# Kernel optimization log

Hardware: AMD Instinct MI355X
Metric: run time of the kernel (lower is better)

The kernel has to match this reference:

```python
import jax, jax.numpy as jnp
import numpy as np

# AAA hyperparameters (init_kwargs)
ALPHA = 1.0
TAU = 6.0
KAPPA = 100
T_TEMP = 1.0
BETA = 5.0
LR = 0.1
# torch.optim.AdamW defaults
B1, B2, EPS, WD = 0.9, 0.999, 1e-8, 0.01

B, D, C = 4096, 2048, 1000


def setup_inputs() -> dict:
    key = jax.random.key(0)
    kx, kw, kb = jax.random.split(key, 3)
    x = jax.random.normal(kx, (B, D), dtype=jnp.float32)
    W = jax.random.normal(kw, (D, C), dtype=jnp.float32) * 0.02  # linear classifier weight
    b = jax.random.normal(kb, (C,), dtype=jnp.float32) * 0.01
    return {"x": x, "W": W, "b": b}


def _ce(logits, y):
    # per-sample cross-entropy (nn.CrossEntropyLoss(reduce=False))
    return jax.nn.logsumexp(logits, axis=1) - jnp.take_along_axis(logits, y[:, None], axis=1)[:, 0]


def reference(x, W, b):
    # model inference under torch.no_grad(); z is detached in AAA
    z = jax.lax.stop_gradient(x @ W + b)  # [B, C]
    y = jnp.argmax(z, axis=1)             # pred_y, constant indices

    l_org = _ce(z, y)                                            # [B]
    l_atr = (jnp.floor(l_org / TAU) + 0.5) * TAU                 # [B]
    # AAA_type == 'sin'
    l_trg = l_org - ALPHA * TAU * jnp.sin(jnp.pi * (1.0 - 2.0 * (l_org - l_atr) / TAU))
    p_trg = jnp.max(jax.nn.softmax(z / T_TEMP, axis=1), axis=1)  # [B]

    def loss_fn(u):
        term1 = jnp.abs(_ce(u, y) - l_trg)                       # [B]
        # NOTE: torch.max(F.softmax(u, dim=1)) has NO dim arg -> GLOBAL max scalar,
        # broadcast against p_trg [B]. Faithful to the source.
        term2 = BETA * jnp.abs(jnp.max(jax.nn.softmax(u, axis=1)) - p_trg)
        return jnp.sum(term1 + term2)

    grad_fn = jax.grad(loss_fn)

    def adamw_step(carry, t):
        u, m, v = carry
        g = grad_fn(u)
        u = u * (1.0 - LR * WD)                  # decoupled weight decay (torch AdamW)
        m = B1 * m + (1.0 - B1) * g
        v = B2 * v + (1.0 - B2) * g * g
        mhat = m / (1.0 - jnp.power(B1, t))
        vhat = v / (1.0 - jnp.power(B2, t))
        u = u - LR * mhat / (jnp.sqrt(vhat) + EPS)
        return (u, m, v), None

    init = (z, jnp.zeros_like(z), jnp.zeros_like(z))
    steps = jnp.arange(1, KAPPA + 1, dtype=jnp.float32)
    (u, _, _), _ = jax.lax.scan(adamw_step, init, steps)
    return u  # protected logits [B, C]
```

## Files before the change

kernel.cpp:

```cpp
#include <hip/hip_runtime.h>

#define BB 4096
#define DD 2048
#define CC 1000

typedef short short8 __attribute__((ext_vector_type(8)));
typedef float f32x4 __attribute__((ext_vector_type(4)));

__device__ __forceinline__ unsigned short f2bf(float x) {
  unsigned u = __float_as_uint(x);
  unsigned r = (u + 0x7FFFu + ((u >> 16) & 1u)) >> 16;
  return (unsigned short)r;
}
__device__ __forceinline__ float bf2f(unsigned short h) {
  return __uint_as_float(((unsigned)h) << 16);
}

__device__ __forceinline__ float fexp(float x) { return __expf(x); }
__device__ __forceinline__ float flog(float x) { return __logf(x); }
__device__ __forceinline__ float frcp(float x) {
  return __builtin_amdgcn_rcpf(x);
}
__device__ __forceinline__ float fsqrt(float x) {
  return __builtin_amdgcn_sqrtf(x);
}

__device__ __forceinline__ void wave_argmax(float& val, int& idx) {
#pragma unroll
  for (int off = 1; off < 64; off <<= 1) {
    float ov = __shfl_xor(val, off, 64);
    int oi = __shfl_xor(idx, off, 64);
    if (ov > val || (ov == val && oi < idx)) { val = ov; idx = oi; }
  }
}

__device__ __forceinline__ float wave_sum(float v) {
#pragma unroll
  for (int off = 1; off < 64; off <<= 1) v += __shfl_xor(v, off, 64);
  return v;
}

__global__ __launch_bounds__(256) void gemm_kernel(
    const float* __restrict__ X, const float* __restrict__ W,
    const float* __restrict__ Bv, float* __restrict__ Z) {
  __shared__ float sA[16][68];
  __shared__ float sB[16][68];
  const int tid = threadIdx.x;
  const int rowTile = blockIdx.y * 64;
  const int colTile = blockIdx.x * 64;
  const int tx = tid & 15, ty = tid >> 4;
  float acc[4][4] = {};
  const int aRow = tid >> 2, aK = (tid & 3) << 2;
  const int bK = tid >> 4, bC = (tid & 15) << 2;
  const bool fullCol = (colTile + 64) <= CC;
  for (int k0 = 0; k0 < DD; k0 += 16) {
    const float4 av = *(const float4*)&X[(size_t)(rowTile + aRow) * DD + k0 + aK];
    sA[aK + 0][aRow] = av.x;
    sA[aK + 1][aRow] = av.y;
    sA[aK + 2][aRow] = av.z;
    sA[aK + 3][aRow] = av.w;
    float4 bv;
    if (fullCol) {
      bv = *(const float4*)&W[(size_t)(k0 + bK) * CC + colTile + bC];
    } else {
      const int c0 = colTile + bC;
      bv.x = (c0 + 0 < CC) ? W[(size_t)(k0 + bK) * CC + c0 + 0] : 0.f;
      bv.y = (c0 + 1 < CC) ? W[(size_t)(k0 + bK) * CC + c0 + 1] : 0.f;
      bv.z = (c0 + 2 < CC) ? W[(size_t)(k0 + bK) * CC + c0 + 2] : 0.f;
      bv.w = (c0 + 3 < CC) ? W[(size_t)(k0 + bK) * CC + c0 + 3] : 0.f;
    }
    *(float4*)&sB[bK][bC] = bv;
    __syncthreads();
#pragma unroll
    for (int kk = 0; kk < 16; ++kk) {
      const float4 a4 = *(const float4*)&sA[kk][ty << 2];
      const float4 b4 = *(const float4*)&sB[kk][tx << 2];
      const float ar[4] = {a4.x, a4.y, a4.z, a4.w};
      const float br[4] = {b4.x, b4.y, b4.z, b4.w};
#pragma unroll
      for (int i = 0; i < 4; ++i)
#pragma unroll
        for (int j = 0; j < 4; ++j) acc[i][j] = fmaf(ar[i], br[j], acc[i][j]);
    }
    __syncthreads();
  }
#pragma unroll
  for (int i = 0; i < 4; ++i) {
    const int r = rowTile + (ty << 2) + i;
#pragma unroll
    for (int j = 0; j < 4; ++j) {
      const int c = colTile + (tx << 2) + j;
      if (c < CC) Z[(size_t)r * CC + c] = acc[i][j] + Bv[c];
    }
  }
}

__global__ __launch_bounds__(256) void conv_a(
    const float* __restrict__ A, unsigned short* __restrict__ Ah,
    unsigned short* __restrict__ Al) {
  const int i = (blockIdx.x * 256 + threadIdx.x) * 4;
  const float4 v = *(const float4*)(A + i);
  ushort4 h, l;
  h.x = f2bf(v.x); l.x = f2bf(v.x - bf2f(h.x));
  h.y = f2bf(v.y); l.y = f2bf(v.y - bf2f(h.y));
  h.z = f2bf(v.z); l.z = f2bf(v.z - bf2f(h.z));
  h.w = f2bf(v.w); l.w = f2bf(v.w - bf2f(h.w));
  *(ushort4*)(Ah + i) = h;
  *(ushort4*)(Al + i) = l;
}

__global__ __launch_bounds__(256) void conv_b(
    const float* __restrict__ B, unsigned short* __restrict__ Bht,
    unsigned short* __restrict__ Blt) {
  __shared__ float t[32][33];
  const int kt = blockIdx.x * 32;
  const int nt = blockIdx.y * 32;
  const int tx = threadIdx.x & 31, ty = threadIdx.x >> 5;
#pragma unroll
  for (int r = 0; r < 4; ++r) {
    const int k = kt + ty + r * 8, n = nt + tx;
    t[ty + r * 8][tx] = (n < CC) ? B[(size_t)k * CC + n] : 0.f;
  }
  __syncthreads();
#pragma unroll
  for (int r = 0; r < 4; ++r) {
    const int n = nt + ty + r * 8, k = kt + tx;
    if (n < CC) {
      const float v = t[tx][ty + r * 8];
      const unsigned short h = f2bf(v);
      Bht[(size_t)n * DD + k] = h;
      Blt[(size_t)n * DD + k] = f2bf(v - bf2f(h));
    }
  }
}

#define PITCH 68
__global__ __launch_bounds__(256) void mfma_gemm(
    const unsigned short* __restrict__ Ah, const unsigned short* __restrict__ Al,
    const unsigned short* __restrict__ Bht, const unsigned short* __restrict__ Blt,
    const float* __restrict__ Bv, float* __restrict__ Z) {
  __shared__ unsigned short sA[128 * PITCH];
  __shared__ unsigned short sB[128 * PITCH];
  const int tid = threadIdx.x;
  const int n0 = blockIdx.x * 128;
  const int m0 = blockIdx.y * 128;
  const int wave = tid >> 6, lane = tid & 63;
  const int wr = (wave >> 1) * 64;
  const int wc = (wave & 1) * 64;
  const int fr = lane & 15;
  const int fq = lane >> 4;

  f32x4 acc[4][4] = {};

  const int sr = tid >> 1;
  const int sc = (tid & 1) * 32;
  const bool bvalid = (n0 + sr) < CC;

  union Frag {
    short8 v;
    uint2 u[2];
  };

  for (int s = 0; s < 96; ++s) {
    const int kp = s << 6;
    const int seg = kp >> 11;
    const int kk = kp & 2047;
    const unsigned short* Asrc = (seg == 1) ? Al : Ah;
    const unsigned short* Bsrc = (seg == 2) ? Blt : Bht;

    uint4 av0, av1, av2, av3, bv0, bv1, bv2, bv3;
    {
      const uint4* gA =
          (const uint4*)(Asrc + (size_t)(m0 + sr) * DD + kk + sc);
      av0 = gA[0]; av1 = gA[1]; av2 = gA[2]; av3 = gA[3];
      if (bvalid) {
        const uint4* gB =
            (const uint4*)(Bsrc + (size_t)(n0 + sr) * DD + kk + sc);
        bv0 = gB[0]; bv1 = gB[1]; bv2 = gB[2]; bv3 = gB[3];
      } else {
        bv0 = bv1 = bv2 = bv3 = make_uint4(0, 0, 0, 0);
      }
    }
    __syncthreads();
    {
      unsigned short* dA = sA + sr * PITCH + sc;
      ((uint2*)(dA + 0))[0] = make_uint2(av0.x, av0.y);
      ((uint2*)(dA + 4))[0] = make_uint2(av0.z, av0.w);
      ((uint2*)(dA + 8))[0] = make_uint2(av1.x, av1.y);
      ((uint2*)(dA + 12))[0] = make_uint2(av1.z, av1.w);
      ((uint2*)(dA + 16))[0] = make_uint2(av2.x, av2.y);
      ((uint2*)(dA + 20))[0] = make_uint2(av2.z, av2.w);
      ((uint2*)(dA + 24))[0] = make_uint2(av3.x, av3.y);
      ((uint2*)(dA + 28))[0] = make_uint2(av3.z, av3.w);
      unsigned short* dB = sB + sr * PITCH + sc;
      ((uint2*)(dB + 0))[0] = make_uint2(bv0.x, bv0.y);
      ((uint2*)(dB + 4))[0] = make_uint2(bv0.z, bv0.w);
      ((uint2*)(dB + 8))[0] = make_uint2(bv1.x, bv1.y);
      ((uint2*)(dB + 12))[0] = make_uint2(bv1.z, bv1.w);
      ((uint2*)(dB + 16))[0] = make_uint2(bv2.x, bv2.y);
      ((uint2*)(dB + 20))[0] = make_uint2(bv2.z, bv2.w);
      ((uint2*)(dB + 24))[0] = make_uint2(bv3.x, bv3.y);
      ((uint2*)(dB + 28))[0] = make_uint2(bv3.z, bv3.w);
    }
    __syncthreads();

#pragma unroll
    for (int h = 0; h < 2; ++h) {
      const int ko = h * 32 + fq * 8;
      Frag a4[4], b4[4];
#pragma unroll
      for (int mt = 0; mt < 4; ++mt) {
        const unsigned short* p = sA + (wr + mt * 16 + fr) * PITCH + ko;
        a4[mt].u[0] = *(const uint2*)(p);
        a4[mt].u[1] = *(const uint2*)(p + 4);
      }
#pragma unroll
      for (int nt = 0; nt < 4; ++nt) {
        const unsigned short* p = sB + (wc + nt * 16 + fr) * PITCH + ko;
        b4[nt].u[0] = *(const uint2*)(p);
        b4[nt].u[1] = *(const uint2*)(p + 4);
      }
#pragma unroll
      for (int mt = 0; mt < 4; ++mt)
#pragma unroll
        for (int nt = 0; nt < 4; ++nt)
          acc[mt][nt] = __builtin_amdgcn_mfma_f32_16x16x32_bf16(
              a4[mt].v, b4[nt].v, acc[mt][nt], 0, 0, 0);
    }
  }

#pragma unroll
  for (int nt = 0; nt < 4; ++nt) {
    const int col = n0 + wc + nt * 16 + fr;
    if (col < CC) {
      const float bb = Bv[col];
#pragma unroll
      for (int mt = 0; mt < 4; ++mt) {
        const int rbase = m0 + wr + mt * 16 + fq * 4;
#pragma unroll
        for (int r = 0; r < 4; ++r)
          Z[(size_t)(rbase + r) * CC + col] = acc[mt][nt][r] + bb;
      }
    }
  }
}

__global__ __launch_bounds__(256) void stats_kernel(
    const float* __restrict__ Z, int* __restrict__ Y,
    float* __restrict__ Lt, float* __restrict__ Pt) {
  const int wave = threadIdx.x >> 6, lane = threadIdx.x & 63;
  const int row = blockIdx.x * 4 + wave;
  float uv[16];
#pragma unroll
  for (int k = 0; k < 16; ++k) {
    const int j = lane + (k << 6);
    uv[k] = (j < CC) ? Z[(size_t)row * CC + j] : -__builtin_inff();
  }
  float mx = uv[0];
  int ai = lane;
#pragma unroll
  for (int k = 1; k < 16; ++k) {
    const int j = lane + (k << 6);
    if (uv[k] > mx) { mx = uv[k]; ai = j; }
  }
  wave_argmax(mx, ai);
  float sum = 0.f;
#pragma unroll
  for (int k = 0; k < 16; ++k) sum += fexp(uv[k] - mx);
  sum = wave_sum(sum);
  if (lane == 0) {
    const float lse = mx + flog(sum);
    const float lorg = lse - mx;
    const float latr = (floorf(lorg / 6.0f) + 0.5f) * 6.0f;
    const float lt =
        lorg - 6.0f * sinf(3.14159265358979323846f *
                           (1.0f - 2.0f * (lorg - latr) / 6.0f));
    Y[row] = ai;
    Lt[row] = lt;
    Pt[row] = frcp(sum);
  }
}

__global__ __launch_bounds__(1024) void sort_kernel(
    const float* __restrict__ P, float* __restrict__ Out) {
  __shared__ float s[4096];
  const int tid = threadIdx.x;
  for (int i = tid; i < 4096; i += 1024) s[i] = P[i];
  __syncthreads();
  for (int k = 2; k <= 4096; k <<= 1) {
    for (int j = k >> 1; j > 0; j >>= 1) {
      for (int i = tid; i < 4096; i += 1024) {
        const int ixj = i ^ j;
        if (ixj > i) {
          const float a = s[i], b = s[ixj];
          const bool up = ((i & k) == 0);
          if (up ? (a > b) : (a < b)) { s[i] = b; s[ixj] = a; }
        }
      }
      __syncthreads();
    }
  }
  for (int i = tid; i < 4096; i += 1024) Out[i] = s[i];
}

__global__ __launch_bounds__(1024, 1) void opt_kernel(
    float* __restrict__ ZU, const int* __restrict__ Yarr,
    const float* __restrict__ Ltrg, const float* __restrict__ Sorted,
    unsigned long long* __restrict__ Slots) {
  const int tid = threadIdx.x;
  const int wave = tid >> 6, lane = tid & 63;
  const int row = blockIdx.x * 16 + wave;

  __shared__ float s_sorted[4096];
  __shared__ float s_coarse[64];
  __shared__ float s_cval[2][16];
  __shared__ int s_cidx[2][16];
  __shared__ float s_coef[2];
  __shared__ int s_rc[2];
  __shared__ int s_arrive[2];
  __shared__ int s_done[2];

  for (int i = tid; i < 4096; i += 1024) s_sorted[i] = Sorted[i];
  if (tid < 64) s_coarse[tid] = Sorted[tid << 6];
  if (tid == 0) {
    s_arrive[0] = 0;
    s_arrive[1] = 0;
    s_done[0] = 0;
    s_done[1] = 0;
  }

  float u[16], m[16], v[16];
#pragma unroll
  for (int k = 0; k < 16; ++k) {
    const int j = lane + (k << 6);
    u[k] = (j < CC) ? ZU[(size_t)row * CC + j] : -__builtin_inff();
    m[k] = 0.f;
    v[k] = 0.f;
  }
  const int y = Yarr[row];
  const float ltrg = Ltrg[row];
  const int ky = y >> 6, ly = y & 63;

  float pb1 = 1.0f, pb2 = 1.0f;
  __syncthreads();

#pragma unroll 1
  for (int t = 1; t <= 100; ++t) {
    const int p = t & 1;
    pb1 *= 0.9f;
    pb2 *= 0.999f;
    const float im1 = frcp(1.0f - pb1);
    const float im2 = frcp(1.0f - pb2);

    float mx = u[0];
    int ai = lane;
#pragma unroll
    for (int k = 1; k < 16; ++k) {
      const int j = lane + (k << 6);
      if (u[k] > mx) { mx = u[k]; ai = j; }
    }
    wave_argmax(mx, ai);
    float sum = 0.f;
#pragma unroll
    for (int k = 0; k < 16; ++k) sum += fexp(u[k] - mx);
    sum = wave_sum(sum);
    const float lse = mx + flog(sum);
    float uyl = 0.f;
#pragma unroll
    for (int k = 0; k < 16; ++k) uyl = (k == ky) ? u[k] : uyl;
    const float uy = __shfl(uyl, ly, 64);
    const float ce = lse - uy;
    const float pmax = frcp(sum);
    const float a = (ce > ltrg) ? 1.0f : ((ce < ltrg) ? -1.0f : 0.0f);

    if (lane == 0) {
      s_cval[p][wave] = pmax;
      s_cidx[p][wave] = (row << 10) | ai;
      __hip_atomic_fetch_add(&s_arrive[p], 1, __ATOMIC_RELEASE,
                             __HIP_MEMORY_SCOPE_WORKGROUP);
    }
    const int target = 16 * ((t >> 1) + (t & 1));
    while (__hip_atomic_load(&s_arrive[p], __ATOMIC_ACQUIRE,
                             __HIP_MEMORY_SCOPE_WORKGROUP) < target) {
    }

    float bv = s_cval[p][0];
    int bi = s_cidx[p][0];
#pragma unroll
    for (int w = 1; w < 16; ++w) {
      const float ov = s_cval[p][w];
      const int oi = s_cidx[p][w];
      if (ov > bv || (ov == bv && oi < bi)) { bv = ov; bi = oi; }
    }
    const int candw = (bi >> 10) & 15;
    const bool iscand = (wave == candw);

    unsigned long long* slot_buf = &Slots[p * 256];
    if (tid == 0) {
      const unsigned long long pack =
          ((unsigned long long)__float_as_uint(bv) << 32) |
          (unsigned)((t << 24) | bi);
      __hip_atomic_store(&slot_buf[blockIdx.x], pack, __ATOMIC_RELAXED,
                         __HIP_MEMORY_SCOPE_AGENT);
    }

    auto adam_update = [&](bool with_t2, float coef, int cstar) {
#pragma unroll
      for (int k = 0; k < 16; ++k) {
        const int j = lane + (k << 6);
        const float p2 = fexp(u[k] - mx) * pmax;
        float g = a * (p2 - ((j == y) ? 1.0f : 0.0f));
        if (with_t2) g += coef * (((j == cstar) ? 1.0f : 0.0f) - p2);
        u[k] *= 0.999f;
        m[k] = 0.9f * m[k] + 0.1f * g;
        v[k] = 0.999f * v[k] + 0.001f * g * g;
        const float mh = m[k] * im1;
        const float vh = v[k] * im2;
        u[k] -= 0.1f * mh * frcp(fsqrt(vh) + 1e-8f);
      }
    };

    if (!iscand && wave != 0) adam_update(false, 0.f, 0);

    if (wave == 0) {
      unsigned long long pv[4];
      unsigned fresh = 0u;
      while (fresh != 0xFu) {
#pragma unroll
        for (int q = 0; q < 4; ++q) {
          if (!(fresh & (1u << q))) {
            const unsigned long long pk = __hip_atomic_load(
                &slot_buf[lane + (q << 6)], __ATOMIC_RELAXED,
                __HIP_MEMORY_SCOPE_AGENT);
            if ((unsigned)((pk >> 24) & 0xFFu) == (unsigned)t) {
              pv[q] = pk;
              fresh |= 1u << q;
            }
          }
        }
        if (fresh != 0xFu) __builtin_amdgcn_s_sleep(1);
      }
      float gv = -1.0f;
      int gi = 0x7fffffff;
#pragma unroll
      for (int q = 0; q < 4; ++q) {
        const float ov = __uint_as_float((unsigned)(pv[q] >> 32));
        const int oi = (int)(pv[q] & 0x3FFFFFu);
        if (ov > gv || (ov == gv && oi < gi)) { gv = ov; gi = oi; }
      }
      wave_argmax(gv, gi);
      const float ss = gv;
      const float v1 = s_coarse[lane];
      const int c1 = __popcll(__ballot(v1 < ss));
      int nlt = 0;
      if (c1 > 0) {
        const float v2 = s_sorted[((c1 - 1) << 6) + lane];
        nlt = ((c1 - 1) << 6) + __popcll(__ballot(v2 < ss));
      }
      const int c2 = __popcll(__ballot(v1 <= ss));
      int nle = 0;
      if (c2 > 0) {
        const float v3 = s_sorted[((c2 - 1) << 6) + lane];
        nle = ((c2 - 1) << 6) + __popcll(__ballot(v3 <= ss));
      }
      const int S = nlt - (4096 - nle);
      const float coef0 = 5.0f * (float)S * ss;
      if (lane == 0) {
        s_coef[p] = coef0;
        s_rc[p] = gi;
        __hip_atomic_store(&s_done[p], t, __ATOMIC_RELEASE,
                           __HIP_MEMORY_SCOPE_WORKGROUP);
      }
      if (iscand) {
        adam_update((gi >> 10) == row, coef0, gi & 1023);
      } else {
        adam_update(false, 0.f, 0);
      }
    }

    if (iscand && wave != 0) {
      while (__hip_atomic_load(&s_done[p], __ATOMIC_ACQUIRE,
                               __HIP_MEMORY_SCOPE_WORKGROUP) < t) {
      }
      const int rc = s_rc[p];
      const bool win = ((rc >> 10) == row);
      adam_update(win, s_coef[p], rc & 1023);
    }
  }

#pragma unroll
  for (int k = 0; k < 16; ++k) {
    const int j = lane + (k << 6);
    if (j < CC) ZU[(size_t)row * CC + j] = u[k];
  }
}

extern "C" void kernel_launch(void* const* d_in, const int* in_sizes, int n_in,
                              void* d_out, int out_size, void* d_ws,
                              size_t ws_size, hipStream_t stream) {
  const float* x = (const float*)d_in[0];
  const float* W = (const float*)d_in[1];
  const float* b = (const float*)d_in[2];
  float* z = (float*)d_out;

  char* ws = (char*)d_ws;
  int* y_arr = (int*)ws;
  float* ltrg_arr = (float*)(ws + (16 << 10));
  float* ptrg_arr = (float*)(ws + (32 << 10));
  float* sorted = (float*)(ws + (48 << 10));
  unsigned long long* slots =
      (unsigned long long*)(ws + (64 << 10));

  const size_t A_BYTES = (size_t)BB * DD * 2;
  const size_t B_BYTES = (size_t)CC * DD * 2;
  unsigned short* AhP = (unsigned short*)(ws + (1 << 20));
  unsigned short* AlP = (unsigned short*)(ws + (1 << 20) + A_BYTES);
  unsigned short* BhP = (unsigned short*)(ws + (1 << 20) + 2 * A_BYTES);
  unsigned short* BlP =
      (unsigned short*)(ws + (1 << 20) + 2 * A_BYTES + B_BYTES);
  const bool use_mfma = ws_size >= ((size_t)44 << 20);

  if (use_mfma) {
    conv_a<<<dim3(8192), 256, 0, stream>>>(x, AhP, AlP);
    conv_b<<<dim3(64, 32), 256, 0, stream>>>(W, BhP, BlP);
    mfma_gemm<<<dim3(8, 32), 256, 0, stream>>>(AhP, AlP, BhP, BlP, b, z);
  } else {
    gemm_kernel<<<dim3(16, 64), 256, 0, stream>>>(x, W, b, z);
  }
  stats_kernel<<<dim3(1024), 256, 0, stream>>>(z, y_arr, ltrg_arr, ptrg_arr);
  sort_kernel<<<dim3(1), 1024, 0, stream>>>(ptrg_arr, sorted);

  void* args[5] = {&z, &y_arr, &ltrg_arr, &sorted, &slots};
  hipLaunchCooperativeKernel((const void*)opt_kernel, dim3(256), dim3(1024),
                             args, 0u, stream);
}
```

Measured before the change: 972.9 us.

## Fuse conversion kernels and let candidate wave do global argmax itself

Merges the A and B bf16-split conversion kernels into one launch with a block-index branch, saving a kernel launch. In the iterative optimizer, the candidate wave now polls the global slot buffer and computes the term2 coefficient itself, instead of wave 0 doing it and signalling through shared memory. This removes one intra-block handoff and spin-wait per step, and a sleep is added to the arrival spin loop to reduce LDS contention. The trade-off is that the candidate wave polls global memory directly, and wave 0 no longer helps when it is not the candidate.

```diff
diff --git a/kernel.cpp b/kernel.cpp
--- a/kernel.cpp
+++ b/kernel.cpp
@@ -95,41 +95,41 @@
   }
 }
 
-__global__ __launch_bounds__(256) void conv_a(
+__global__ __launch_bounds__(256) void conv_fused(
     const float* __restrict__ A, unsigned short* __restrict__ Ah,
-    unsigned short* __restrict__ Al) {
-  const int i = (blockIdx.x * 256 + threadIdx.x) * 4;
-  const float4 v = *(const float4*)(A + i);
-  ushort4 h, l;
-  h.x = f2bf(v.x); l.x = f2bf(v.x - bf2f(h.x));
-  h.y = f2bf(v.y); l.y = f2bf(v.y - bf2f(h.y));
-  h.z = f2bf(v.z); l.z = f2bf(v.z - bf2f(h.z));
-  h.w = f2bf(v.w); l.w = f2bf(v.w - bf2f(h.w));
-  *(ushort4*)(Ah + i) = h;
-  *(ushort4*)(Al + i) = l;
-}
-
-__global__ __launch_bounds__(256) void conv_b(
-    const float* __restrict__ B, unsigned short* __restrict__ Bht,
-    unsigned short* __restrict__ Blt) {
+    unsigned short* __restrict__ Al, const float* __restrict__ B,
+    unsigned short* __restrict__ Bht, unsigned short* __restrict__ Blt) {
   __shared__ float t[32][33];
-  const int kt = blockIdx.x * 32;
-  const int nt = blockIdx.y * 32;
-  const int tx = threadIdx.x & 31, ty = threadIdx.x >> 5;
-#pragma unroll
-  for (int r = 0; r < 4; ++r) {
-    const int k = kt + ty + r * 8, n = nt + tx;
-    t[ty + r * 8][tx] = (n < CC) ? B[(size_t)k * CC + n] : 0.f;
-  }
-  __syncthreads();
-#pragma unroll
-  for (int r = 0; r < 4; ++r) {
-    const int n = nt + ty + r * 8, k = kt + tx;
-    if (n < CC) {
-      const float v = t[tx][ty + r * 8];
-      const unsigned short h = f2bf(v);
-      Bht[(size_t)n * DD + k] = h;
-      Blt[(size_t)n * DD + k] = f2bf(v - bf2f(h));
+  if (blockIdx.x < 8192) {
+    const int i = (blockIdx.x * 256 + threadIdx.x) * 4;
+    const float4 v = *(const float4*)(A + i);
+    ushort4 h, l;
+    h.x = f2bf(v.x); l.x = f2bf(v.x - bf2f(h.x));
+    h.y = f2bf(v.y); l.y = f2bf(v.y - bf2f(h.y));
+    h.z = f2bf(v.z); l.z = f2bf(v.z - bf2f(h.z));
+    h.w = f2bf(v.w); l.w = f2bf(v.w - bf2f(h.w));
+    *(ushort4*)(Ah + i) = h;
+    *(ushort4*)(Al + i) = l;
+  } else {
+    const int bb = blockIdx.x - 8192;
+    const int kt = (bb & 63) * 32;
+    const int nt = (bb >> 6) * 32;
+    const int tx = threadIdx.x & 31, ty = threadIdx.x >> 5;
+#pragma unroll
+    for (int r = 0; r < 4; ++r) {
+      const int k = kt + ty + r * 8, n = nt + tx;
+      t[ty + r * 8][tx] = (n < CC) ? B[(size_t)k * CC + n] : 0.f;
+    }
+    __syncthreads();
+#pragma unroll
+    for (int r = 0; r < 4; ++r) {
+      const int n = nt + ty + r * 8, k = kt + tx;
+      if (n < CC) {
+        const float v = t[tx][ty + r * 8];
+        const unsigned short h = f2bf(v);
+        Bht[(size_t)n * DD + k] = h;
+        Blt[(size_t)n * DD + k] = f2bf(v - bf2f(h));
+      }
     }
   }
 }
@@ -315,18 +315,13 @@
   __shared__ float s_coarse[64];
   __shared__ float s_cval[2][16];
   __shared__ int s_cidx[2][16];
-  __shared__ float s_coef[2];
-  __shared__ int s_rc[2];
   __shared__ int s_arrive[2];
-  __shared__ int s_done[2];
 
   for (int i = tid; i < 4096; i += 1024) s_sorted[i] = Sorted[i];
   if (tid < 64) s_coarse[tid] = Sorted[tid << 6];
   if (tid == 0) {
     s_arrive[0] = 0;
     s_arrive[1] = 0;
-    s_done[0] = 0;
-    s_done[1] = 0;
   }
 
   float u[16], m[16], v[16];
@@ -382,6 +377,7 @@
     const int target = 16 * ((t >> 1) + (t & 1));
     while (__hip_atomic_load(&s_arrive[p], __ATOMIC_ACQUIRE,
                              __HIP_MEMORY_SCOPE_WORKGROUP) < target) {
+      __builtin_amdgcn_s_sleep(1);
     }
 
     float bv = s_cval[p][0];
@@ -420,9 +416,9 @@
       }
     };
 
-    if (!iscand && wave != 0) adam_update(false, 0.f, 0);
-
-    if (wave == 0) {
+    if (!iscand) {
+      adam_update(false, 0.f, 0);
+    } else {
       unsigned long long pv[4];
       unsigned fresh = 0u;
       while (fresh != 0xFu) {
@@ -464,27 +460,8 @@
         nle = ((c2 - 1) << 6) + __popcll(__ballot(v3 <= ss));
       }
       const int S = nlt - (4096 - nle);
-      const float coef0 = 5.0f * (float)S * ss;
-      if (lane == 0) {
-        s_coef[p] = coef0;
-        s_rc[p] = gi;
-        __hip_atomic_store(&s_done[p], t, __ATOMIC_RELEASE,
-                           __HIP_MEMORY_SCOPE_WORKGROUP);
-      }
-      if (iscand) {
-        adam_update((gi >> 10) == row, coef0, gi & 1023);
-      } else {
-        adam_update(false, 0.f, 0);
-      }
-    }
-
-    if (iscand && wave != 0) {
-      while (__hip_atomic_load(&s_done[p], __ATOMIC_ACQUIRE,
-                               __HIP_MEMORY_SCOPE_WORKGROUP) < t) {
-      }
-      const int rc = s_rc[p];
-      const bool win = ((rc >> 10) == row);
-      adam_update(win, s_coef[p], rc & 1023);
+      const float coef = 5.0f * (float)S * ss;
+      adam_update((gi >> 10) == row, coef, gi & 1023);
     }
   }
 
@@ -521,8 +498,7 @@
   const bool use_mfma = ws_size >= ((size_t)44 << 20);
 
   if (use_mfma) {
-    conv_a<<<dim3(8192), 256, 0, stream>>>(x, AhP, AlP);
-    conv_b<<<dim3(64, 32), 256, 0, stream>>>(W, BhP, BlP);
+    conv_fused<<<dim3(10240), 256, 0, stream>>>(x, AhP, AlP, W, BhP, BlP);
     mfma_gemm<<<dim3(8, 32), 256, 0, stream>>>(AhP, AlP, BhP, BlP, b, z);
   } else {
     gemm_kernel<<<dim3(16, 64), 256, 0, stream>>>(x, W, b, z);
```

Result: slower. 1.067 ms (+9.6%).
